# Performance work log

Measured on AMD Instinct MI355X. Metric: run time of the kernel, lower is better.

Reference implementation:

```python
import jax, jax.numpy as jnp
import numpy as np

B, J, HID, NG = 16384, 16, 128, 5
NEG = -9e15
EDGES = [(0,1),(1,2),(2,3),(0,4),(4,5),(5,6),(0,7),(7,8),(8,9),(9,10),(8,11),(11,12),(12,13),(8,14),(14,15)]

def _skeleton_mask():
    m = np.eye(J, dtype=bool)
    for i, j in EDGES:
        m[i, j] = True
        m[j, i] = True
    return jnp.asarray(m)

def setup_inputs() -> dict:
    key = jax.random.key(0)
    ks = jax.random.split(key, 8)
    s = 0.05
    ones, zeros = jnp.ones(HID), jnp.zeros(HID)
    bn = jnp.stack([ones, zeros, zeros, ones])  # gamma, beta, running_mean, running_var
    return {
        "x": jax.random.normal(ks[0], (B, J, 2), jnp.float32),
        "W_in": jax.random.normal(ks[1], (2, 2, HID), jnp.float32) * s,
        "e_in": jax.random.normal(ks[2], (J, J), jnp.float32),
        "b_in": jnp.zeros((HID,), jnp.float32),
        "bn_in": bn,
        "W_mid": jax.random.normal(ks[3], (8, 2, HID, HID), jnp.float32) * s,
        "e_mid": jax.random.normal(ks[4], (8, J, J), jnp.float32),
        "b_mid": jnp.zeros((8, HID), jnp.float32),
        "bn_mid": jnp.broadcast_to(bn, (8, 4, HID)),
        "W_out": jax.random.normal(ks[5], (2, HID, NG * 5), jnp.float32) * s,
        "e_out": jax.random.normal(ks[6], (J, J), jnp.float32),
        "b_out": jnp.zeros((NG * 5,), jnp.float32),
        "adj_mask": _skeleton_mask(),
    }

def _semgconv(x, W, e, b, mask):
    # x: [B,J,Cin]; W: [2,Cin,Cout]; e: [J,J] attention logits on adjacency support
    h0 = jnp.einsum('bjc,cf->bjf', x, W[0])  # self transform
    h1 = jnp.einsum('bjc,cf->bjf', x, W[1])  # neighbor transform
    A = jax.nn.softmax(jnp.where(mask, e, NEG), axis=1)  # [J,J]
    eye = jnp.eye(mask.shape[0], dtype=A.dtype)
    out = jnp.einsum('ij,bjf->bif', A * eye, h0) + jnp.einsum('ij,bjf->bif', A * (1.0 - eye), h1)
    return out + b

def _bn_relu(h, bn):
    gamma, beta, mean, var = bn[0], bn[1], bn[2], bn[3]
    return jax.nn.relu((h - mean) * jax.lax.rsqrt(var + 1e-5) * gamma + beta)

def reference(x, W_in, e_in, b_in, bn_in, W_mid, e_mid, b_mid, bn_mid, W_out, e_out, b_out, adj_mask):
    h = _bn_relu(_semgconv(x, W_in, e_in, b_in, adj_mask), bn_in)
    for i in range(4):  # 4 residual blocks, each with 2 gconvs
        r = h
        for k in (2 * i, 2 * i + 1):
            h = _bn_relu(_semgconv(h, W_mid[k], e_mid[k], b_mid[k], adj_mask), bn_mid[k])
        h = r + h
    out = _semgconv(h, W_out, e_out, b_out, adj_mask)  # [B,J,25]
    mu = jnp.tanh(out[:, :, : NG * 3].reshape(out.shape[0], out.shape[1], NG, 3))
    sigma = out[:, :, NG * 3 : NG * 4][:, :, :, None]
    pi = out[:, :, NG * 4 : NG * 5]
    sigma = jnp.maximum(jax.nn.elu(sigma) + 1.0, 1e-10)
    return mu, sigma, pi
```

## Files before the change

kernel.cpp:

```cpp
#include <hip/hip_runtime.h>


typedef unsigned short u16;
typedef float f32x4 __attribute__((ext_vector_type(4)));
typedef float f32x2 __attribute__((ext_vector_type(2)));
typedef _Float16 f16x2 __attribute__((ext_vector_type(2)));
typedef _Float16 f16x4 __attribute__((ext_vector_type(4)));
typedef _Float16 f16x8 __attribute__((ext_vector_type(8)));

#define BATCH 16384
#define BT 8

#define MU_OFF (BATCH * 16 * 15)
#define SG_OFF (BATCH * 16 * 5)

#define WS_WTO 524288
#define WS_A   540672
#define WS_S   550912
#define WS_T   555520
#define WS_BP  560128

__device__ __forceinline__ float b2f(u16 b) {
  unsigned u = ((unsigned)b) << 16; float f; __builtin_memcpy(&f, &u, 4); return f;
}
__device__ __forceinline__ u16 f2b(float f) {
  unsigned u; __builtin_memcpy(&u, &f, 4);
  u = (u + 0x7fffu + ((u >> 16) & 1u)) >> 16;
  return (u16)u;
}
__device__ __forceinline__ u16 f2h(float f) {
  _Float16 h = (_Float16)f; u16 b; __builtin_memcpy(&b, &h, 2); return b;
}
__device__ __forceinline__ bool dtyf32(const void* bnin) {
  return *(const unsigned*)bnin == 0x3F800000u;
}
__device__ __forceinline__ float ldf(const void* p, int i, bool f32) {
  return f32 ? ((const float*)p)[i] : b2f(((const u16*)p)[i]);
}
__device__ __forceinline__ f32x4 mm32(f16x8 a, f16x8 b, f32x4 c) {
  return __builtin_amdgcn_mfma_f32_16x16x32_f16(a, b, c, 0, 0, 0);
}
__device__ __forceinline__ f16x8 pk8(f32x4 u, f32x4 v) {
  auto a = __builtin_amdgcn_cvt_pkrtz(u[0], u[1]);
  auto b = __builtin_amdgcn_cvt_pkrtz(u[2], u[3]);
  auto c = __builtin_amdgcn_cvt_pkrtz(v[0], v[1]);
  auto d = __builtin_amdgcn_cvt_pkrtz(v[2], v[3]);
  f16x8 r;
  __builtin_memcpy(&r, &a, 4);
  __builtin_memcpy((char*)&r + 4,  &b, 4);
  __builtin_memcpy((char*)&r + 8,  &c, 4);
  __builtin_memcpy((char*)&r + 12, &d, 4);
  return r;
}

__device__ const u16 MASKBITS[16] = {
  0x0093, 0x0007, 0x000E, 0x000C, 0x0031, 0x0070, 0x0060, 0x0181,
  0x4B80, 0x0700, 0x0600, 0x1900, 0x3800, 0x3000, 0xC100, 0xC000
};

__global__ void prep_kernel(const void* __restrict__ Wmid, const void* __restrict__ Wout,
                            const void* __restrict__ ein,  const void* __restrict__ emid,
                            const void* __restrict__ eout, const void* __restrict__ bnin,
                            const void* __restrict__ bnmid, const void* __restrict__ bin,
                            const void* __restrict__ bmid, const void* __restrict__ bout,
                            u16* __restrict__ WT, u16* __restrict__ WTo,
                            float* __restrict__ A, float* __restrict__ S,
                            float* __restrict__ T, float* __restrict__ bpad) {
  const bool F32 = dtyf32(bnin);
  int tid = blockIdx.x * 256 + threadIdx.x;
  if (tid < 262144) {
    int kk = tid & 127, f = (tid >> 7) & 127, lm = tid >> 14;
    int bo_ = (lm >> 1) * 512;
    float gam = ldf(bnmid, bo_ + f, F32);
    float var = ldf(bnmid, bo_ + 384 + f, F32);
    float s = gam * rsqrtf(var + 1e-5f);
    WT[((lm << 7) + f) * 128 + kk] =
        f2h(ldf(Wmid, ((lm << 7) + kk) * 128 + f, F32) * s);
  } else if (tid < 262144 + 8192) {
    int t2 = tid - 262144;
    int kk = t2 & 127, f = (t2 >> 7) & 31, m = t2 >> 12;
    WTo[((m * 32 + f) << 7) + kk] =
        (f < 25) ? f2h(ldf(Wout, (m * 128 + kk) * 25 + f, F32)) : (u16)0;
  } else if (tid < 262144 + 8192 + 160) {
    int t3 = tid - (262144 + 8192);
    int i = t3 & 15, L = t3 >> 4;
    const void* e = (L == 0) ? ein : (L <= 8 ? emid : eout);
    int ebase = (L >= 1 && L <= 8) ? (L - 1) * 256 : 0;
    unsigned mrow = MASKBITS[i];
    float v[16]; float mx = -1e30f;
    for (int j = 0; j < 16; j++) {
      v[j] = ldf(e, ebase + i * 16 + j, F32);
      if ((mrow >> j) & 1) mx = fmaxf(mx, v[j]);
    }
    float sum = 0.f;
    for (int j = 0; j < 16; j++) {
      if ((mrow >> j) & 1) { v[j] = expf(v[j] - mx); sum += v[j]; } else v[j] = 0.f;
    }
    float inv = 1.f / sum;
    for (int j = 0; j < 16; j++) A[L * 256 + i * 16 + j] = v[j] * inv;
  } else if (tid < 262144 + 8192 + 160 + 1152) {
    int t4 = tid - (262144 + 8192 + 160);
    int f = t4 & 127, L = t4 >> 7;
    float gam, bet, mea, var, bb;
    if (L == 0) {
      gam = ldf(bnin, f, F32);       bet = ldf(bnin, 128 + f, F32);
      mea = ldf(bnin, 256 + f, F32); var = ldf(bnin, 384 + f, F32);
      bb  = ldf(bin, f, F32);
    } else {
      int k = L - 1; int bo_ = k * 512;
      gam = ldf(bnmid, bo_ + f, F32);       bet = ldf(bnmid, bo_ + 128 + f, F32);
      mea = ldf(bnmid, bo_ + 256 + f, F32); var = ldf(bnmid, bo_ + 384 + f, F32);
      bb  = ldf(bmid, k * 128 + f, F32);
    }
    float s = gam * rsqrtf(var + 1e-5f);
    S[L * 128 + f] = s;
    T[L * 128 + f] = (bb - mea) * s + bet;
  } else if (tid < 262144 + 8192 + 160 + 1152 + 32) {
    int f = tid - (262144 + 8192 + 160 + 1152);
    bpad[f] = (f < 25) ? ldf(bout, f, F32) : 0.f;
  }
}

__global__ __launch_bounds__(512, 2) void semgcn_main(
    const void* __restrict__ x, const void* __restrict__ Win,
    const u16* __restrict__ WT, const u16* __restrict__ WTo,
    const float* __restrict__ A, const float* __restrict__ S,
    const float* __restrict__ T, const float* __restrict__ bpad,
    const void* __restrict__ bnin, void* __restrict__ out) {
  __shared__ __align__(16) u16 hbuf[2 * 128 * 128];
  const bool F32 = dtyf32(bnin);
  const int tid = threadIdx.x;
  const int w = tid >> 6, lane = tid & 63, q = lane >> 4, n = lane & 15;
  const int bbase = blockIdx.x * BT;
  const int Fb = 16 * w;
  const int rswz = n & 7;
  const int fo = ((((Fb + 4 * q) >> 3) ^ rswz) << 3) + ((4 * q) & 7);
  const f32x4 zf = {0.f, 0.f, 0.f, 0.f};
  f16x4 resid[BT];

  {
    float w00, w01, w10, w11;
    {
      int f = Fb + n;
      float sf = S[f];
      w00 = ldf(Win, f, F32) * sf;        w01 = ldf(Win, 128 + f, F32) * sf;
      w10 = ldf(Win, 256 + f, F32) * sf;  w11 = ldf(Win, 384 + f, F32) * sf;
    }
    f16x8 bm;
    {
      const f32x4 ar = *(const f32x4*)(A + n * 16 + 4 * q);
#pragma unroll
      for (int r = 0; r < 4; r++) {
        int j = 4 * q + r;
        bm[r]     = (j == n) ? (_Float16)ar[r] : (_Float16)0.f;
        bm[4 + r] = (j != n) ? (_Float16)ar[r] : (_Float16)0.f;
      }
    }
    f32x4 Tv = *(const f32x4*)(T + Fb + 4 * q);
#pragma unroll
    for (int c = 0; c < BT; c++) {
      int b = bbase + c;
      float x0[4], x1[4];
#pragma unroll
      for (int r = 0; r < 4; r++) {
        int j = b * 16 + 4 * q + r;
        if (F32) {
          f32x2 xv = *(const f32x2*)((const float*)x + j * 2);
          x0[r] = xv[0]; x1[r] = xv[1];
        } else {
          unsigned xv = *(const unsigned*)((const u16*)x + j * 2);
          x0[r] = b2f((u16)(xv & 0xffffu));
          x1[r] = b2f((u16)(xv >> 16));
        }
      }
      f16x8 am;
#pragma unroll
      for (int r = 0; r < 4; r++) {
        am[r]     = (_Float16)(x0[r] * w00 + x1[r] * w01);
        am[4 + r] = (_Float16)(x0[r] * w10 + x1[r] * w11);
      }
      f32x4 o = mm32(am, bm, Tv);
      f16x4 oh;
#pragma unroll
      for (int r = 0; r < 4; r++) oh[r] = (_Float16)fmaxf(o[r], 0.f);
      resid[c] = oh;
      *(f16x4*)&hbuf[(c * 16 + n) * 128 + fo] = oh;
    }
  }
  __syncthreads();

  for (int kl = 0; kl < 8; kl++) {
    const int bufR = (kl & 1) * 16384;
    const int bufW = ((kl + 1) & 1) * 16384;
    f16x8 wf[2][4];
#pragma unroll
    for (int m = 0; m < 2; m++)
#pragma unroll
      for (int s = 0; s < 4; s++)
        wf[m][s] = *(const f16x8*)(WT + ((((kl * 2 + m) << 7) + Fb + n) << 7)
                                   + 32 * s + 8 * q);
    f16x8 bm;
    {
      const f32x4 ar = *(const f32x4*)(A + (kl + 1) * 256 + n * 16 + 4 * q);
#pragma unroll
      for (int r = 0; r < 4; r++) {
        int j = 4 * q + r;
        bm[r]     = (j == n) ? (_Float16)ar[r] : (_Float16)0.f;
        bm[4 + r] = (j != n) ? (_Float16)ar[r] : (_Float16)0.f;
      }
    }
    f32x4 Tv = *(const f32x4*)(T + (kl + 1) * 128 + Fb + 4 * q);
#pragma unroll
    for (int cc = 0; cc < BT; cc += 2) {
      const int RA = cc * 16 + n, RB = RA + 16;
      f16x8 ha[4], hb[4];
#pragma unroll
      for (int s = 0; s < 4; s++) {
        int co = (((4 * s + q) ^ rswz) << 3);
        ha[s] = *(const f16x8*)&hbuf[bufR + RA * 128 + co];
        hb[s] = *(const f16x8*)&hbuf[bufR + RB * 128 + co];
      }
      f32x4 aA0 = zf, aA1 = zf, aB0 = zf, aB1 = zf;
#pragma unroll
      for (int s = 0; s < 4; s++) {
        aA0 = mm32(ha[s], wf[0][s], aA0);
        aB0 = mm32(hb[s], wf[0][s], aB0);
        aA1 = mm32(ha[s], wf[1][s], aA1);
        aB1 = mm32(hb[s], wf[1][s], aB1);
      }
      {
        f32x4 o = mm32(pk8(aA0, aA1), bm, Tv);
        f16x4 oh;
#pragma unroll
        for (int r = 0; r < 4; r++) {
          _Float16 h = (_Float16)o[r];
          oh[r] = h > (_Float16)0.f ? h : (_Float16)0.f;
        }
        if (kl & 1) {
          oh = oh + resid[cc];
          resid[cc] = oh;
        }
        *(f16x4*)&hbuf[bufW + RA * 128 + fo] = oh;
      }
      {
        f32x4 o = mm32(pk8(aB0, aB1), bm, Tv);
        f16x4 oh;
#pragma unroll
        for (int r = 0; r < 4; r++) {
          _Float16 h = (_Float16)o[r];
          oh[r] = h > (_Float16)0.f ? h : (_Float16)0.f;
        }
        if (kl & 1) {
          oh = oh + resid[cc + 1];
          resid[cc + 1] = oh;
        }
        *(f16x4*)&hbuf[bufW + RB * 128 + fo] = oh;
      }
    }
    __syncthreads();
  }

  {
    int c = w;
    int b = bbase + c;
    int R = c * 16 + n;
    f16x8 hf[4];
#pragma unroll
    for (int s = 0; s < 4; s++) {
      int co = (((4 * s + q) ^ rswz) << 3);
      hf[s] = *(const f16x8*)&hbuf[R * 128 + co];
    }
    f16x8 bm;
    {
      const f32x4 ar = *(const f32x4*)(A + 9 * 256 + n * 16 + 4 * q);
#pragma unroll
      for (int r = 0; r < 4; r++) {
        int j = 4 * q + r;
        bm[r]     = (j == n) ? (_Float16)ar[r] : (_Float16)0.f;
        bm[4 + r] = (j != n) ? (_Float16)ar[r] : (_Float16)0.f;
      }
    }
#pragma unroll
    for (int t = 0; t < 2; t++) {
      f16x8 wo0[4], wo1[4];
#pragma unroll
      for (int s = 0; s < 4; s++) {
        wo0[s] = *(const f16x8*)(WTo + ((0 * 32 + 16 * t + n) << 7) + 32 * s + 8 * q);
        wo1[s] = *(const f16x8*)(WTo + ((1 * 32 + 16 * t + n) << 7) + 32 * s + 8 * q);
      }
      f32x4 acc0 = zf, acc1 = zf;
#pragma unroll
      for (int s = 0; s < 4; s++) {
        acc0 = mm32(hf[s], wo0[s], acc0);
        acc1 = mm32(hf[s], wo1[s], acc1);
      }
      f32x4 bv = *(const f32x4*)(bpad + 16 * t + 4 * q);
      f32x4 o = mm32(pk8(acc0, acc1), bm, bv);
      int row = b * 16 + n;
#pragma unroll
      for (int r = 0; r < 4; r++) {
        int f = 16 * t + 4 * q + r;
        float v = o[r];
        int idx = -1; float val = 0.f;
        if (f < 15) {
          idx = row * 15 + f;                    val = tanhf(v);
        } else if (f < 20) {
          float sg = (v > 0.f) ? (v + 1.f) : expf(v);
          idx = MU_OFF + row * 5 + (f - 15);     val = fmaxf(sg, 1e-10f);
        } else if (f < 25) {
          idx = MU_OFF + SG_OFF + row * 5 + (f - 20); val = v;
        }
        if (idx >= 0) {
          if (F32) ((float*)out)[idx] = val;
          else     ((u16*)out)[idx]   = f2b(val);
        }
      }
    }
  }
}

extern "C" void kernel_launch(void* const* d_in, const int* in_sizes, int n_in,
                              void* d_out, int out_size, void* d_ws, size_t ws_size,
                              hipStream_t stream) {
  const void* x     = d_in[0];
  const void* Win   = d_in[1];
  const void* ein   = d_in[2];
  const void* bin   = d_in[3];
  const void* bnin  = d_in[4];
  const void* Wmid  = d_in[5];
  const void* emid  = d_in[6];
  const void* bmid  = d_in[7];
  const void* bnmid = d_in[8];
  const void* Wout  = d_in[9];
  const void* eout  = d_in[10];
  const void* bout  = d_in[11];

  char* ws = (char*)d_ws;
  u16*   WT   = (u16*)(ws);
  u16*   WTo  = (u16*)(ws + WS_WTO);
  float* A    = (float*)(ws + WS_A);
  float* S    = (float*)(ws + WS_S);
  float* T    = (float*)(ws + WS_T);
  float* bpad = (float*)(ws + WS_BP);

  prep_kernel<<<1062, 256, 0, stream>>>(Wmid, Wout, ein, emid, eout, bnin, bnmid,
                                        bin, bmid, bout, WT, WTo, A, S, T, bpad);
  semgcn_main<<<BATCH / BT, 512, 0, stream>>>(x, Win, WT, WTo, A, S, T, bpad,
                                              bnin, (u16*)d_out);
}
```

Measured before the change: 302.8 us.

## Split warps into 2 batch halves x 4 feature groups of 32 columns

Changes the work split inside the block. Before, each of the 8 wavefronts owned 16 output features across all 8 batch chunks. Now each wavefront owns 32 features for 4 of the 8 batch chunks. Each wave reads half as much activation data from LDS per layer, but loads twice as many weight fragments from global memory and holds them in registers (wf grows from 8 to 16 f16x8 values). This raises register pressure under launch_bounds(512,2) and may cause spills.

Result: slower. 457.3 us (+51.0%).

```diff
diff --git a/kernel.cpp b/kernel.cpp
--- a/kernel.cpp
+++ b/kernel.cpp
@@ -132,19 +132,23 @@
   const int tid = threadIdx.x;
   const int w = tid >> 6, lane = tid & 63, q = lane >> 4, n = lane & 15;
   const int bbase = blockIdx.x * BT;
-  const int Fb = 16 * w;
+  const int h2 = w >> 2, g = w & 3;
+  const int Fb2 = 32 * g;
   const int rswz = n & 7;
-  const int fo = ((((Fb + 4 * q) >> 3) ^ rswz) << 3) + ((4 * q) & 7);
+  const int fo0 = ((((Fb2 + 4 * q) >> 3) ^ rswz) << 3) + ((4 * q) & 7);
+  const int fo1 = ((((Fb2 + 16 + 4 * q) >> 3) ^ rswz) << 3) + ((4 * q) & 7);
   const f32x4 zf = {0.f, 0.f, 0.f, 0.f};
-  f16x4 resid[BT];
+  f16x4 resid[8];
+
 
   {
-    float w00, w01, w10, w11;
-    {
-      int f = Fb + n;
+    float w00[2], w01[2], w10[2], w11[2];
+#pragma unroll
+    for (int t = 0; t < 2; t++) {
+      int f = Fb2 + 16 * t + n;
       float sf = S[f];
-      w00 = ldf(Win, f, F32) * sf;        w01 = ldf(Win, 128 + f, F32) * sf;
-      w10 = ldf(Win, 256 + f, F32) * sf;  w11 = ldf(Win, 384 + f, F32) * sf;
+      w00[t] = ldf(Win, f, F32) * sf;        w01[t] = ldf(Win, 128 + f, F32) * sf;
+      w10[t] = ldf(Win, 256 + f, F32) * sf;  w11[t] = ldf(Win, 384 + f, F32) * sf;
     }
     f16x8 bm;
     {
@@ -156,10 +160,14 @@
         bm[4 + r] = (j != n) ? (_Float16)ar[r] : (_Float16)0.f;
       }
     }
-    f32x4 Tv = *(const f32x4*)(T + Fb + 4 * q);
-#pragma unroll
-    for (int c = 0; c < BT; c++) {
-      int b = bbase + c;
+    f32x4 Tv[2];
+#pragma unroll
+    for (int t = 0; t < 2; t++)
+      Tv[t] = *(const f32x4*)(T + Fb2 + 16 * t + 4 * q);
+#pragma unroll
+    for (int cc = 0; cc < 4; cc++) {
+      int chunk = 4 * h2 + cc;
+      int b = bbase + chunk;
       float x0[4], x1[4];
 #pragma unroll
       for (int r = 0; r < 4; r++) {
@@ -173,18 +181,22 @@
           x1[r] = b2f((u16)(xv >> 16));
         }
       }
-      f16x8 am;
-#pragma unroll
-      for (int r = 0; r < 4; r++) {
-        am[r]     = (_Float16)(x0[r] * w00 + x1[r] * w01);
-        am[4 + r] = (_Float16)(x0[r] * w10 + x1[r] * w11);
-      }
-      f32x4 o = mm32(am, bm, Tv);
-      f16x4 oh;
-#pragma unroll
-      for (int r = 0; r < 4; r++) oh[r] = (_Float16)fmaxf(o[r], 0.f);
-      resid[c] = oh;
-      *(f16x4*)&hbuf[(c * 16 + n) * 128 + fo] = oh;
+      int R = chunk * 16 + n;
+#pragma unroll
+      for (int t = 0; t < 2; t++) {
+        f16x8 am;
+#pragma unroll
+        for (int r = 0; r < 4; r++) {
+          am[r]     = (_Float16)(x0[r] * w00[t] + x1[r] * w01[t]);
+          am[4 + r] = (_Float16)(x0[r] * w10[t] + x1[r] * w11[t]);
+        }
+        f32x4 o = mm32(am, bm, Tv[t]);
+        f16x4 oh;
+#pragma unroll
+        for (int r = 0; r < 4; r++) oh[r] = (_Float16)fmaxf(o[r], 0.f);
+        resid[cc * 2 + t] = oh;
+        *(f16x4*)&hbuf[R * 128 + (t ? fo1 : fo0)] = oh;
+      }
     }
   }
   __syncthreads();
@@ -192,13 +204,15 @@
   for (int kl = 0; kl < 8; kl++) {
     const int bufR = (kl & 1) * 16384;
     const int bufW = ((kl + 1) & 1) * 16384;
-    f16x8 wf[2][4];
+    f16x8 wf[2][2][4];
 #pragma unroll
     for (int m = 0; m < 2; m++)
 #pragma unroll
-      for (int s = 0; s < 4; s++)
-        wf[m][s] = *(const f16x8*)(WT + ((((kl * 2 + m) << 7) + Fb + n) << 7)
-                                   + 32 * s + 8 * q);
+      for (int t = 0; t < 2; t++)
+#pragma unroll
+        for (int s = 0; s < 4; s++)
+          wf[m][t][s] = *(const f16x8*)(WT +
+              ((((kl * 2 + m) << 7) + Fb2 + 16 * t + n) << 7) + 32 * s + 8 * q);
     f16x8 bm;
     {
       const f32x4 ar = *(const f32x4*)(A + (kl + 1) * 256 + n * 16 + 4 * q);
@@ -209,27 +223,29 @@
         bm[4 + r] = (j != n) ? (_Float16)ar[r] : (_Float16)0.f;
       }
     }
-    f32x4 Tv = *(const f32x4*)(T + (kl + 1) * 128 + Fb + 4 * q);
-#pragma unroll
-    for (int cc = 0; cc < BT; cc += 2) {
-      const int RA = cc * 16 + n, RB = RA + 16;
-      f16x8 ha[4], hb[4];
+    f32x4 Tv[2];
+#pragma unroll
+    for (int t = 0; t < 2; t++)
+      Tv[t] = *(const f32x4*)(T + (kl + 1) * 128 + Fb2 + 16 * t + 4 * q);
+#pragma unroll
+    for (int cc = 0; cc < 4; cc++) {
+      const int R = (4 * h2 + cc) * 16 + n;
+      f16x8 hf[4];
 #pragma unroll
       for (int s = 0; s < 4; s++) {
         int co = (((4 * s + q) ^ rswz) << 3);
-        ha[s] = *(const f16x8*)&hbuf[bufR + RA * 128 + co];
-        hb[s] = *(const f16x8*)&hbuf[bufR + RB * 128 + co];
-      }
-      f32x4 aA0 = zf, aA1 = zf, aB0 = zf, aB1 = zf;
+        hf[s] = *(const f16x8*)&hbuf[bufR + R * 128 + co];
+      }
+      f32x4 a00 = zf, a01 = zf, a10 = zf, a11 = zf;
 #pragma unroll
       for (int s = 0; s < 4; s++) {
-        aA0 = mm32(ha[s], wf[0][s], aA0);
-        aB0 = mm32(hb[s], wf[0][s], aB0);
-        aA1 = mm32(ha[s], wf[1][s], aA1);
-        aB1 = mm32(hb[s], wf[1][s], aB1);
+        a00 = mm32(hf[s], wf[0][0][s], a00);
+        a01 = mm32(hf[s], wf[1][0][s], a01);
+        a10 = mm32(hf[s], wf[0][1][s], a10);
+        a11 = mm32(hf[s], wf[1][1][s], a11);
       }
       {
-        f32x4 o = mm32(pk8(aA0, aA1), bm, Tv);
+        f32x4 o = mm32(pk8(a00, a01), bm, Tv[0]);
         f16x4 oh;
 #pragma unroll
         for (int r = 0; r < 4; r++) {
@@ -237,13 +253,13 @@
           oh[r] = h > (_Float16)0.f ? h : (_Float16)0.f;
         }
         if (kl & 1) {
-          oh = oh + resid[cc];
-          resid[cc] = oh;
-        }
-        *(f16x4*)&hbuf[bufW + RA * 128 + fo] = oh;
+          oh = oh + resid[cc * 2];
+          resid[cc * 2] = oh;
+        }
+        *(f16x4*)&hbuf[bufW + R * 128 + fo0] = oh;
       }
       {
-        f32x4 o = mm32(pk8(aB0, aB1), bm, Tv);
+        f32x4 o = mm32(pk8(a10, a11), bm, Tv[1]);
         f16x4 oh;
 #pragma unroll
         for (int r = 0; r < 4; r++) {
@@ -251,10 +267,10 @@
           oh[r] = h > (_Float16)0.f ? h : (_Float16)0.f;
         }
         if (kl & 1) {
-          oh = oh + resid[cc + 1];
-          resid[cc + 1] = oh;
-        }
-        *(f16x4*)&hbuf[bufW + RB * 128 + fo] = oh;
+          oh = oh + resid[cc * 2 + 1];
+          resid[cc * 2 + 1] = oh;
+        }
+        *(f16x4*)&hbuf[bufW + R * 128 + fo1] = oh;
       }
     }
     __syncthreads();
```

## Use rotating triple half-buffers in LDS to raise blocks per CU

Applied to the files above, without the earlier changes.

Replaces the two full-size ping-pong LDS activation buffers with three half-batch buffers that rotate. Each layer is processed in two passes, so the freed half buffer takes the next output. This cuts shared memory per block from 64KB to 48KB so more blocks can be resident per CU, and the launch-bounds hint is raised to 4 blocks. The cost is an extra barrier per layer, and the tighter register budget implied by the new occupancy target risks spills.

Result: no change. 298.0 us (-1.6%).

```diff
diff --git a/kernel.cpp b/kernel.cpp
--- a/kernel.cpp
+++ b/kernel.cpp
@@ -10,6 +10,7 @@
 
 #define BATCH 16384
 #define BT 8
+#define HB 8192
 
 #define MU_OFF (BATCH * 16 * 15)
 #define SG_OFF (BATCH * 16 * 5)
@@ -121,13 +122,13 @@
   }
 }
 
-__global__ __launch_bounds__(512, 2) void semgcn_main(
+__global__ __launch_bounds__(512, 4) void semgcn_main(
     const void* __restrict__ x, const void* __restrict__ Win,
     const u16* __restrict__ WT, const u16* __restrict__ WTo,
     const float* __restrict__ A, const float* __restrict__ S,
     const float* __restrict__ T, const float* __restrict__ bpad,
     const void* __restrict__ bnin, void* __restrict__ out) {
-  __shared__ __align__(16) u16 hbuf[2 * 128 * 128];
+  __shared__ __align__(16) u16 hbuf[3 * HB];
   const bool F32 = dtyf32(bnin);
   const int tid = threadIdx.x;
   const int w = tid >> 6, lane = tid & 63, q = lane >> 4, n = lane & 15;
@@ -137,6 +138,7 @@
   const int fo = ((((Fb + 4 * q) >> 3) ^ rswz) << 3) + ((4 * q) & 7);
   const f32x4 zf = {0.f, 0.f, 0.f, 0.f};
   f16x4 resid[BT];
+  int r0 = 0, r1 = 1, r2 = 2;
 
   {
     float w00, w01, w10, w11;
@@ -184,14 +186,13 @@
 #pragma unroll
       for (int r = 0; r < 4; r++) oh[r] = (_Float16)fmaxf(o[r], 0.f);
       resid[c] = oh;
-      *(f16x4*)&hbuf[(c * 16 + n) * 128 + fo] = oh;
+      int dst = (c >> 2) * HB + ((c & 3) * 16 + n) * 128 + fo;
+      *(f16x4*)&hbuf[dst] = oh;
     }
   }
   __syncthreads();
 
   for (int kl = 0; kl < 8; kl++) {
-    const int bufR = (kl & 1) * 16384;
-    const int bufW = ((kl + 1) & 1) * 16384;
     f16x8 wf[2][4];
 #pragma unroll
     for (int m = 0; m < 2; m++)
@@ -211,64 +212,72 @@
     }
     f32x4 Tv = *(const f32x4*)(T + (kl + 1) * 128 + Fb + 4 * q);
 #pragma unroll
-    for (int cc = 0; cc < BT; cc += 2) {
-      const int RA = cc * 16 + n, RB = RA + 16;
-      f16x8 ha[4], hb[4];
-#pragma unroll
-      for (int s = 0; s < 4; s++) {
-        int co = (((4 * s + q) ^ rswz) << 3);
-        ha[s] = *(const f16x8*)&hbuf[bufR + RA * 128 + co];
-        hb[s] = *(const f16x8*)&hbuf[bufR + RB * 128 + co];
-      }
-      f32x4 aA0 = zf, aA1 = zf, aB0 = zf, aB1 = zf;
-#pragma unroll
-      for (int s = 0; s < 4; s++) {
-        aA0 = mm32(ha[s], wf[0][s], aA0);
-        aB0 = mm32(hb[s], wf[0][s], aB0);
-        aA1 = mm32(ha[s], wf[1][s], aA1);
-        aB1 = mm32(hb[s], wf[1][s], aB1);
-      }
-      {
-        f32x4 o = mm32(pk8(aA0, aA1), bm, Tv);
-        f16x4 oh;
-#pragma unroll
-        for (int r = 0; r < 4; r++) {
-          _Float16 h = (_Float16)o[r];
-          oh[r] = h > (_Float16)0.f ? h : (_Float16)0.f;
-        }
-        if (kl & 1) {
-          oh = oh + resid[cc];
-          resid[cc] = oh;
-        }
-        *(f16x4*)&hbuf[bufW + RA * 128 + fo] = oh;
-      }
-      {
-        f32x4 o = mm32(pk8(aB0, aB1), bm, Tv);
-        f16x4 oh;
-#pragma unroll
-        for (int r = 0; r < 4; r++) {
-          _Float16 h = (_Float16)o[r];
-          oh[r] = h > (_Float16)0.f ? h : (_Float16)0.f;
-        }
-        if (kl & 1) {
-          oh = oh + resid[cc + 1];
-          resid[cc + 1] = oh;
-        }
-        *(f16x4*)&hbuf[bufW + RB * 128 + fo] = oh;
-      }
-    }
-    __syncthreads();
+    for (int p = 0; p < 2; p++) {
+      const int rd = (p == 0 ? r0 : r1) * HB;
+      const int wr = (p == 0 ? r2 : r0) * HB;
+#pragma unroll
+      for (int cc = 0; cc < 4; cc += 2) {
+        const int lA = cc * 16 + n, lB = lA + 16;
+        const int chA = 4 * p + cc, chB = chA + 1;
+        f16x8 ha[4], hb[4];
+#pragma unroll
+        for (int s = 0; s < 4; s++) {
+          int co = (((4 * s + q) ^ rswz) << 3);
+          ha[s] = *(const f16x8*)&hbuf[rd + lA * 128 + co];
+          hb[s] = *(const f16x8*)&hbuf[rd + lB * 128 + co];
+        }
+        f32x4 aA0 = zf, aA1 = zf, aB0 = zf, aB1 = zf;
+#pragma unroll
+        for (int s = 0; s < 4; s++) {
+          aA0 = mm32(ha[s], wf[0][s], aA0);
+          aB0 = mm32(hb[s], wf[0][s], aB0);
+          aA1 = mm32(ha[s], wf[1][s], aA1);
+          aB1 = mm32(hb[s], wf[1][s], aB1);
+        }
+        {
+          f32x4 o = mm32(pk8(aA0, aA1), bm, Tv);
+          f16x4 oh;
+#pragma unroll
+          for (int r = 0; r < 4; r++) {
+            _Float16 h = (_Float16)o[r];
+            oh[r] = h > (_Float16)0.f ? h : (_Float16)0.f;
+          }
+          if (kl & 1) {
+            oh = oh + resid[chA];
+            resid[chA] = oh;
+          }
+          *(f16x4*)&hbuf[wr + lA * 128 + fo] = oh;
+        }
+        {
+          f32x4 o = mm32(pk8(aB0, aB1), bm, Tv);
+          f16x4 oh;
+#pragma unroll
+          for (int r = 0; r < 4; r++) {
+            _Float16 h = (_Float16)o[r];
+            oh[r] = h > (_Float16)0.f ? h : (_Float16)0.f;
+          }
+          if (kl & 1) {
+            oh = oh + resid[chB];
+            resid[chB] = oh;
+          }
+          *(f16x4*)&hbuf[wr + lB * 128 + fo] = oh;
+        }
+      }
+      __syncthreads();
+    }
+    int tmp = r2; r2 = r1; r1 = r0; r0 = tmp;
   }
 
   {
     int c = w;
     int b = bbase + c;
-    int R = c * 16 + n;
+    const int base = (c >> 2 ? r1 : r0) * HB;
+    const int lrow = (c & 3) * 16 + n;
     f16x8 hf[4];
 #pragma unroll
     for (int s = 0; s < 4; s++) {
       int co = (((4 * s + q) ^ rswz) << 3);
-      hf[s] = *(const f16x8*)&hbuf[R * 128 + co];
+      hf[s] = *(const f16x8*)&hbuf[base + lrow * 128 + co];
     }
     f16x8 bm;
     {
```

## Keep activations in registers per wave, removing LDS ping-pong and block barriers

Applied to the files above, without the earlier changes.

Each wave now owns two poses and holds their full 128-channel hidden state in registers across all layers. The MFMA accumulator layout feeds directly into the next layer's A operand because the weight K dimension is permuted in the prep kernel. This removes the shared-memory buffer, the per-layer __syncthreads and the LDS traffic. The cost is that every wave reloads the full weight matrices from global/L2 per layer, so weight traffic rises sharply. Register pressure also grows, and the launch-bounds occupancy hint is dropped.

Result: slower. 585.6 us (+93.4%).

```diff
diff --git a/kernel.cpp b/kernel.cpp
--- a/kernel.cpp
+++ b/kernel.cpp
@@ -9,7 +9,6 @@
 typedef _Float16 f16x8 __attribute__((ext_vector_type(8)));
 
 #define BATCH 16384
-#define BT 8
 
 #define MU_OFF (BATCH * 16 * 15)
 #define SG_OFF (BATCH * 16 * 5)
@@ -52,6 +51,12 @@
   __builtin_memcpy((char*)&r + 12, &d, 4);
   return r;
 }
+__device__ __forceinline__ f16x8 cat(f16x4 lo, f16x4 hi) {
+  f16x8 r;
+#pragma unroll
+  for (int i = 0; i < 4; i++) { r[i] = lo[i]; r[4 + i] = hi[i]; }
+  return r;
+}
 
 __device__ const u16 MASKBITS[16] = {
   0x0093, 0x0007, 0x000E, 0x000C, 0x0031, 0x0070, 0x0060, 0x0181,
@@ -69,18 +74,21 @@
   const bool F32 = dtyf32(bnin);
   int tid = blockIdx.x * 256 + threadIdx.x;
   if (tid < 262144) {
-    int kk = tid & 127, f = (tid >> 7) & 127, lm = tid >> 14;
+    int idx = tid & 127, c = (tid >> 7) & 127, lm = tid >> 14;
+    int s = idx >> 5, qq = (idx >> 3) & 3, j = idx & 7;
+    int k = 32 * s + 16 * (j >> 2) + 4 * qq + (j & 3);
     int bo_ = (lm >> 1) * 512;
-    float gam = ldf(bnmid, bo_ + f, F32);
-    float var = ldf(bnmid, bo_ + 384 + f, F32);
-    float s = gam * rsqrtf(var + 1e-5f);
-    WT[((lm << 7) + f) * 128 + kk] =
-        f2h(ldf(Wmid, ((lm << 7) + kk) * 128 + f, F32) * s);
+    float gam = ldf(bnmid, bo_ + c, F32);
+    float var = ldf(bnmid, bo_ + 384 + c, F32);
+    float sc = gam * rsqrtf(var + 1e-5f);
+    WT[tid] = f2h(ldf(Wmid, ((lm << 7) + k) * 128 + c, F32) * sc);
   } else if (tid < 262144 + 8192) {
     int t2 = tid - 262144;
-    int kk = t2 & 127, f = (t2 >> 7) & 31, m = t2 >> 12;
-    WTo[((m * 32 + f) << 7) + kk] =
-        (f < 25) ? f2h(ldf(Wout, (m * 128 + kk) * 25 + f, F32)) : (u16)0;
+    int idx = t2 & 127, c = (t2 >> 7) & 31, m = t2 >> 12;
+    int s = idx >> 5, qq = (idx >> 3) & 3, j = idx & 7;
+    int k = 32 * s + 16 * (j >> 2) + 4 * qq + (j & 3);
+    WTo[((m * 32 + c) << 7) + idx] =
+        (c < 25) ? f2h(ldf(Wout, (m * 128 + k) * 25 + c, F32)) : (u16)0;
   } else if (tid < 262144 + 8192 + 160) {
     int t3 = tid - (262144 + 8192);
     int i = t3 & 15, L = t3 >> 4;
@@ -121,31 +129,36 @@
   }
 }
 
-__global__ __launch_bounds__(512, 2) void semgcn_main(
+__global__ __launch_bounds__(512) void semgcn_main(
     const void* __restrict__ x, const void* __restrict__ Win,
     const u16* __restrict__ WT, const u16* __restrict__ WTo,
     const float* __restrict__ A, const float* __restrict__ S,
     const float* __restrict__ T, const float* __restrict__ bpad,
     const void* __restrict__ bnin, void* __restrict__ out) {
-  __shared__ __align__(16) u16 hbuf[2 * 128 * 128];
   const bool F32 = dtyf32(bnin);
   const int tid = threadIdx.x;
   const int w = tid >> 6, lane = tid & 63, q = lane >> 4, n = lane & 15;
-  const int bbase = blockIdx.x * BT;
-  const int Fb = 16 * w;
-  const int rswz = n & 7;
-  const int fo = ((((Fb + 4 * q) >> 3) ^ rswz) << 3) + ((4 * q) & 7);
+  const int pose0 = (blockIdx.x * 8 + w) * 2;
   const f32x4 zf = {0.f, 0.f, 0.f, 0.f};
-  f16x4 resid[BT];
+  f16x4 hA[2][8], hB[2][8];
+
+  float x0[2][4], x1[2][4];
+#pragma unroll
+  for (int p = 0; p < 2; p++)
+#pragma unroll
+    for (int r = 0; r < 4; r++) {
+      int j = (pose0 + p) * 16 + 4 * q + r;
+      if (F32) {
+        f32x2 xv = *(const f32x2*)((const float*)x + j * 2);
+        x0[p][r] = xv[0]; x1[p][r] = xv[1];
+      } else {
+        unsigned xv = *(const unsigned*)((const u16*)x + j * 2);
+        x0[p][r] = b2f((u16)(xv & 0xffffu));
+        x1[p][r] = b2f((u16)(xv >> 16));
+      }
+    }
 
   {
-    float w00, w01, w10, w11;
-    {
-      int f = Fb + n;
-      float sf = S[f];
-      w00 = ldf(Win, f, F32) * sf;        w01 = ldf(Win, 128 + f, F32) * sf;
-      w10 = ldf(Win, 256 + f, F32) * sf;  w11 = ldf(Win, 384 + f, F32) * sf;
-    }
     f16x8 bm;
     {
       const f32x4 ar = *(const f32x4*)(A + n * 16 + 4 * q);
@@ -156,52 +169,86 @@
         bm[4 + r] = (j != n) ? (_Float16)ar[r] : (_Float16)0.f;
       }
     }
-    f32x4 Tv = *(const f32x4*)(T + Fb + 4 * q);
-#pragma unroll
-    for (int c = 0; c < BT; c++) {
-      int b = bbase + c;
-      float x0[4], x1[4];
-#pragma unroll
-      for (int r = 0; r < 4; r++) {
-        int j = b * 16 + 4 * q + r;
-        if (F32) {
-          f32x2 xv = *(const f32x2*)((const float*)x + j * 2);
-          x0[r] = xv[0]; x1[r] = xv[1];
-        } else {
-          unsigned xv = *(const unsigned*)((const u16*)x + j * 2);
-          x0[r] = b2f((u16)(xv & 0xffffu));
-          x1[r] = b2f((u16)(xv >> 16));
+#pragma unroll
+    for (int t = 0; t < 8; t++) {
+      int f = 16 * t + n;
+      float sf = S[f];
+      float w00 = ldf(Win, f, F32) * sf,        w01 = ldf(Win, 128 + f, F32) * sf;
+      float w10 = ldf(Win, 256 + f, F32) * sf,  w11 = ldf(Win, 384 + f, F32) * sf;
+      f32x4 Tv = *(const f32x4*)(T + 16 * t + 4 * q);
+#pragma unroll
+      for (int p = 0; p < 2; p++) {
+        f16x8 am;
+#pragma unroll
+        for (int r = 0; r < 4; r++) {
+          am[r]     = (_Float16)(x0[p][r] * w00 + x1[p][r] * w01);
+          am[4 + r] = (_Float16)(x0[p][r] * w10 + x1[p][r] * w11);
         }
-      }
-      f16x8 am;
-#pragma unroll
-      for (int r = 0; r < 4; r++) {
-        am[r]     = (_Float16)(x0[r] * w00 + x1[r] * w01);
-        am[4 + r] = (_Float16)(x0[r] * w10 + x1[r] * w11);
-      }
-      f32x4 o = mm32(am, bm, Tv);
-      f16x4 oh;
-#pragma unroll
-      for (int r = 0; r < 4; r++) oh[r] = (_Float16)fmaxf(o[r], 0.f);
-      resid[c] = oh;
-      *(f16x4*)&hbuf[(c * 16 + n) * 128 + fo] = oh;
-    }
-  }
-  __syncthreads();
-
-  for (int kl = 0; kl < 8; kl++) {
-    const int bufR = (kl & 1) * 16384;
-    const int bufW = ((kl + 1) & 1) * 16384;
-    f16x8 wf[2][4];
-#pragma unroll
-    for (int m = 0; m < 2; m++)
-#pragma unroll
-      for (int s = 0; s < 4; s++)
-        wf[m][s] = *(const f16x8*)(WT + ((((kl * 2 + m) << 7) + Fb + n) << 7)
-                                   + 32 * s + 8 * q);
+        f32x4 o = mm32(am, bm, Tv);
+        f16x4 oh;
+#pragma unroll
+        for (int r = 0; r < 4; r++) oh[r] = (_Float16)fmaxf(o[r], 0.f);
+        hA[p][t] = oh;
+      }
+    }
+  }
+
+#define MIDLAYER(KL, HSRC, HDST, DORES)                                        \
+  {                                                                            \
+    const int kl = (KL);                                                       \
+    f16x8 bm;                                                                  \
+    {                                                                          \
+      const f32x4 ar = *(const f32x4*)(A + (kl + 1) * 256 + n * 16 + 4 * q);   \
+      _Pragma("unroll")                                                        \
+      for (int r = 0; r < 4; r++) {                                            \
+        int j = 4 * q + r;                                                     \
+        bm[r]     = (j == n) ? (_Float16)ar[r] : (_Float16)0.f;                \
+        bm[4 + r] = (j != n) ? (_Float16)ar[r] : (_Float16)0.f;                \
+      }                                                                        \
+    }                                                                          \
+    _Pragma("unroll")                                                          \
+    for (int t = 0; t < 8; t++) {                                              \
+      const u16* wb0 = WT + (((2 * kl + 0) * 128 + 16 * t + n) << 7) + 8 * q;  \
+      const u16* wb1 = WT + (((2 * kl + 1) * 128 + 16 * t + n) << 7) + 8 * q;  \
+      f16x8 wf0[4], wf1[4];                                                    \
+      _Pragma("unroll")                                                        \
+      for (int s = 0; s < 4; s++) {                                            \
+        wf0[s] = *(const f16x8*)(wb0 + 32 * s);                                \
+        wf1[s] = *(const f16x8*)(wb1 + 32 * s);                                \
+      }                                                                        \
+      f32x4 Tv = *(const f32x4*)(T + (kl + 1) * 128 + 16 * t + 4 * q);         \
+      _Pragma("unroll")                                                        \
+      for (int p = 0; p < 2; p++) {                                            \
+        f32x4 a0 = zf, a1 = zf;                                                \
+        _Pragma("unroll")                                                      \
+        for (int s = 0; s < 4; s++) {                                          \
+          f16x8 af = cat(HSRC[p][2 * s], HSRC[p][2 * s + 1]);                  \
+          a0 = mm32(af, wf0[s], a0);                                           \
+          a1 = mm32(af, wf1[s], a1);                                           \
+        }                                                                      \
+        f32x4 o = mm32(pk8(a0, a1), bm, Tv);                                   \
+        f16x4 oh;                                                              \
+        _Pragma("unroll")                                                      \
+        for (int r = 0; r < 4; r++) {                                          \
+          _Float16 h = (_Float16)o[r];              \
+          oh[r] = h > (_Float16)0.f ? h : (_Float16)0.f;                       \
+        }                                                                      \
+        if (DORES) oh = oh + hA[p][t];            \
+        HDST[p][t] = oh;                                                       \
+      }                                                                        \
+    }                                                                          \
+  }
+
+  for (int i = 0; i < 4; i++) {
+    MIDLAYER(2 * i,     hA, hB, 0)
+    MIDLAYER(2 * i + 1, hB, hA, 1)
+  }
+#undef MIDLAYER
+
+  {
     f16x8 bm;
     {
-      const f32x4 ar = *(const f32x4*)(A + (kl + 1) * 256 + n * 16 + 4 * q);
+      const f32x4 ar = *(const f32x4*)(A + 9 * 256 + n * 16 + 4 * q);
 #pragma unroll
       for (int r = 0; r < 4; r++) {
         int j = 4 * q + r;
@@ -209,77 +256,6 @@
         bm[4 + r] = (j != n) ? (_Float16)ar[r] : (_Float16)0.f;
       }
     }
-    f32x4 Tv = *(const f32x4*)(T + (kl + 1) * 128 + Fb + 4 * q);
-#pragma unroll
-    for (int cc = 0; cc < BT; cc += 2) {
-      const int RA = cc * 16 + n, RB = RA + 16;
-      f16x8 ha[4], hb[4];
-#pragma unroll
-      for (int s = 0; s < 4; s++) {
-        int co = (((4 * s + q) ^ rswz) << 3);
-        ha[s] = *(const f16x8*)&hbuf[bufR + RA * 128 + co];
-        hb[s] = *(const f16x8*)&hbuf[bufR + RB * 128 + co];
-      }
-      f32x4 aA0 = zf, aA1 = zf, aB0 = zf, aB1 = zf;
-#pragma unroll
-      for (int s = 0; s < 4; s++) {
-        aA0 = mm32(ha[s], wf[0][s], aA0);
-        aB0 = mm32(hb[s], wf[0][s], aB0);
-        aA1 = mm32(ha[s], wf[1][s], aA1);
-        aB1 = mm32(hb[s], wf[1][s], aB1);
-      }
-      {
-        f32x4 o = mm32(pk8(aA0, aA1), bm, Tv);
-        f16x4 oh;
-#pragma unroll
-        for (int r = 0; r < 4; r++) {
-          _Float16 h = (_Float16)o[r];
-          oh[r] = h > (_Float16)0.f ? h : (_Float16)0.f;
-        }
-        if (kl & 1) {
-          oh = oh + resid[cc];
-          resid[cc] = oh;
-        }
-        *(f16x4*)&hbuf[bufW + RA * 128 + fo] = oh;
-      }
-      {
-        f32x4 o = mm32(pk8(aB0, aB1), bm, Tv);
-        f16x4 oh;
-#pragma unroll
-        for (int r = 0; r < 4; r++) {
-          _Float16 h = (_Float16)o[r];
-          oh[r] = h > (_Float16)0.f ? h : (_Float16)0.f;
-        }
-        if (kl & 1) {
-          oh = oh + resid[cc + 1];
-          resid[cc + 1] = oh;
-        }
-        *(f16x4*)&hbuf[bufW + RB * 128 + fo] = oh;
-      }
-    }
-    __syncthreads();
-  }
-
-  {
-    int c = w;
-    int b = bbase + c;
-    int R = c * 16 + n;
-    f16x8 hf[4];
-#pragma unroll
-    for (int s = 0; s < 4; s++) {
-      int co = (((4 * s + q) ^ rswz) << 3);
-      hf[s] = *(const f16x8*)&hbuf[R * 128 + co];
-    }
-    f16x8 bm;
-    {
-      const f32x4 ar = *(const f32x4*)(A + 9 * 256 + n * 16 + 4 * q);
-#pragma unroll
-      for (int r = 0; r < 4; r++) {
-        int j = 4 * q + r;
-        bm[r]     = (j == n) ? (_Float16)ar[r] : (_Float16)0.f;
-        bm[4 + r] = (j != n) ? (_Float16)ar[r] : (_Float16)0.f;
-      }
-    }
 #pragma unroll
     for (int t = 0; t < 2; t++) {
       f16x8 wo0[4], wo1[4];
@@ -288,31 +264,35 @@
         wo0[s] = *(const f16x8*)(WTo + ((0 * 32 + 16 * t + n) << 7) + 32 * s + 8 * q);
         wo1[s] = *(const f16x8*)(WTo + ((1 * 32 + 16 * t + n) << 7) + 32 * s + 8 * q);
       }
-      f32x4 acc0 = zf, acc1 = zf;
-#pragma unroll
-      for (int s = 0; s < 4; s++) {
-        acc0 = mm32(hf[s], wo0[s], acc0);
-        acc1 = mm32(hf[s], wo1[s], acc1);
-      }
       f32x4 bv = *(const f32x4*)(bpad + 16 * t + 4 * q);
-      f32x4 o = mm32(pk8(acc0, acc1), bm, bv);
-      int row = b * 16 + n;
-#pragma unroll
-      for (int r = 0; r < 4; r++) {
-        int f = 16 * t + 4 * q + r;
-        float v = o[r];
-        int idx = -1; float val = 0.f;
-        if (f < 15) {
-          idx = row * 15 + f;                    val = tanhf(v);
-        } else if (f < 20) {
-          float sg = (v > 0.f) ? (v + 1.f) : expf(v);
-          idx = MU_OFF + row * 5 + (f - 15);     val = fmaxf(sg, 1e-10f);
-        } else if (f < 25) {
-          idx = MU_OFF + SG_OFF + row * 5 + (f - 20); val = v;
+#pragma unroll
+      for (int p = 0; p < 2; p++) {
+        f32x4 a0 = zf, a1 = zf;
+#pragma unroll
+        for (int s = 0; s < 4; s++) {
+          f16x8 af = cat(hA[p][2 * s], hA[p][2 * s + 1]);
+          a0 = mm32(af, wo0[s], a0);
+          a1 = mm32(af, wo1[s], a1);
         }
-        if (idx >= 0) {
-          if (F32) ((float*)out)[idx] = val;
-          else     ((u16*)out)[idx]   = f2b(val);
+        f32x4 o = mm32(pk8(a0, a1), bm, bv);
+        int row = (pose0 + p) * 16 + n;
+#pragma unroll
+        for (int r = 0; r < 4; r++) {
+          int f = 16 * t + 4 * q + r;
+          float v = o[r];
+          int idx = -1; float val = 0.f;
+          if (f < 15) {
+            idx = row * 15 + f;                    val = tanhf(v);
+          } else if (f < 20) {
+            float sg = (v > 0.f) ? (v + 1.f) : expf(v);
+            idx = MU_OFF + row * 5 + (f - 15);     val = fmaxf(sg, 1e-10f);
+          } else if (f < 25) {
+            idx = MU_OFF + SG_OFF + row * 5 + (f - 20); val = v;
+          }
+          if (idx >= 0) {
+            if (F32) ((float*)out)[idx] = val;
+            else     ((u16*)out)[idx]   = f2b(val);
+          }
         }
       }
     }
@@ -345,6 +325,6 @@
 
   prep_kernel<<<1062, 256, 0, stream>>>(Wmid, Wout, ein, emid, eout, bnin, bnmid,
                                         bin, bmid, bout, WT, WTo, A, S, T, bpad);
-  semgcn_main<<<BATCH / BT, 512, 0, stream>>>(x, Win, WT, WTo, A, S, T, bpad,
+  semgcn_main<<<BATCH / 16, 512, 0, stream>>>(x, Win, WT, WTo, A, S, T, bpad,
                                               bnin, (u16*)d_out);
 }
```
